# Kernel tuning notes

Measured on AMD Instinct MI355X. Metric: run time of the kernel, lower is better.

The kernel has to match this reference:

```python
import jax, jax.numpy as jnp
import numpy as np

NUM_HEAD = 8
HIDDEN = 1024


def setup_inputs() -> dict:
    key = jax.random.key(0)
    ks = jax.random.split(key, 7)
    B, Q, K = 2, 256, 256
    return {
        "query": jax.random.normal(ks[0], (B, Q, HIDDEN), jnp.float32),
        "keys": jax.random.normal(ks[1], (B, K, HIDDEN), jnp.float32),
        "values": jax.random.normal(ks[2], (B, K, HIDDEN), jnp.float32),
        "mask": jax.random.randint(ks[3], (B, K), 0, 2, jnp.int32),
        "W_q": jax.random.normal(ks[4], (HIDDEN, HIDDEN), jnp.float32),
        "W_k": jax.random.normal(ks[5], (HIDDEN, HIDDEN), jnp.float32),
        "V_a": jax.random.normal(ks[6], (HIDDEN,), jnp.float32),
    }


def reference(query, keys, values, mask, W_q, W_k, V_a):
    B, Q, H = query.shape
    K = keys.shape[1]
    h_q = query @ W_q                                   # [B,Q,H]
    h_k = keys @ W_k                                    # [B,K,H]
    # additive (Bahdanau) scores, split hidden into heads and sum per head
    h = jnp.tanh(h_q[:, :, None, :] + h_k[:, None, :, :]) * V_a   # [B,Q,K,H]
    logits = h.reshape(B, Q, K, NUM_HEAD, H // NUM_HEAD).sum(-1)  # [B,Q,K,h]
    logits = jnp.transpose(logits, (0, 3, 1, 2))        # [B,h,Q,K]
    penalty = (1.0 - mask.astype(jnp.float32)) * 99.0   # [B,K]
    logits = logits - penalty[:, None, None, :]
    weights = jax.nn.softmax(logits, axis=-1)           # [B,h,Q,K]
    v = values.reshape(B, K, NUM_HEAD, H // NUM_HEAD)   # [B,K,h,d]
    ctx = jnp.einsum('bhqk,bkhd->bqhd', weights, v).reshape(B, Q, H)
    return ctx, weights
```

## Files before the change

### kernel.cpp

```cpp
#include <hip/hip_runtime.h>
#include <hip/hip_bf16.h>


#define TANH_SCALE 2.88539008177792681472f
#define LOG2E      1.44269504088896340736f
#define UCLAMP     13.0f

typedef __attribute__((ext_vector_type(8))) short bf16x8_t;
typedef __attribute__((ext_vector_type(4))) float f32x4_t;

__device__ inline ushort bf16_rne(float f) {
  unsigned u = __float_as_uint(f);
  u += 0x7FFFu + ((u >> 16) & 1u);
  return (ushort)(u >> 16);
}
__device__ inline float bf16_to_f(ushort h) { return __uint_as_float((unsigned)h << 16); }
__device__ inline void split1(float v, ushort& hi, ushort& lo) {
  hi = bf16_rne(v);
  lo = bf16_rne(v - bf16_to_f(hi));
}
__device__ inline float pow8c(float u) {
  u = fminf(u, UCLAMP);
  float u2 = u * u;
  float u4 = u2 * u2;
  return u4 * u4;
}

__global__ __launch_bounds__(256) void prep(
    const float* __restrict__ query, const float* __restrict__ keys,
    const float* __restrict__ Wq, const float* __restrict__ Wk,
    ushort* __restrict__ qhi, ushort* __restrict__ qlo,
    ushort* __restrict__ khi, ushort* __restrict__ klo,
    ushort* __restrict__ wqthi, ushort* __restrict__ wqtlo,
    ushort* __restrict__ wkthi, ushort* __restrict__ wktlo)
{
  __shared__ float t[64][65];
  const int bid = blockIdx.x, tid = threadIdx.x;
  if (bid < 1024) {
    const int z = bid >> 9;
    const float* in = z ? keys : query;
    ushort* hi = z ? khi : qhi;
    ushort* lo = z ? klo : qlo;
    const size_t i = ((size_t)(bid & 511) * 256 + tid) * 4;
    float4 v = *(const float4*)(in + i);
    ushort h0, h1, h2, h3, l0, l1, l2, l3;
    split1(v.x, h0, l0); split1(v.y, h1, l1);
    split1(v.z, h2, l2); split1(v.w, h3, l3);
    *(ushort4*)(hi + i) = make_ushort4(h0, h1, h2, h3);
    *(ushort4*)(lo + i) = make_ushort4(l0, l1, l2, l3);
  } else {
    const int idx = bid - 1024;
    const int z = idx >> 8;
    const float* W = z ? Wk : Wq;
    ushort* thi = z ? wkthi : wqthi;
    ushort* tlo = z ? wktlo : wqtlo;
    const int n0 = (idx & 15) * 64, h0 = ((idx >> 4) & 15) * 64;
    const int r = tid >> 4, c = (tid & 15) * 4;
#pragma unroll
    for (int i = 0; i < 4; ++i) {
      const int rr = r + i * 16;
      float4 wv = *(const float4*)(W + (size_t)(h0 + rr) * 1024 + n0 + c);
      t[rr][c + 0] = wv.x; t[rr][c + 1] = wv.y;
      t[rr][c + 2] = wv.z; t[rr][c + 3] = wv.w;
    }
    __syncthreads();
#pragma unroll
    for (int i = 0; i < 4; ++i) {
      const int rr = r + i * 16;
      ushort h0v, h1v, h2v, h3v, l0v, l1v, l2v, l3v;
      split1(t[c + 0][rr] * TANH_SCALE, h0v, l0v);
      split1(t[c + 1][rr] * TANH_SCALE, h1v, l1v);
      split1(t[c + 2][rr] * TANH_SCALE, h2v, l2v);
      split1(t[c + 3][rr] * TANH_SCALE, h3v, l3v);
      *(ushort4*)(thi + (size_t)(n0 + rr) * 1024 + h0 + c) = make_ushort4(h0v, h1v, h2v, h3v);
      *(ushort4*)(tlo + (size_t)(n0 + rr) * 1024 + h0 + c) = make_ushort4(l0v, l1v, l2v, l3v);
    }
  }
}

__global__ __launch_bounds__(256) void gemm_mfma(
    const ushort* __restrict__ qhi, const ushort* __restrict__ qlo,
    const ushort* __restrict__ khi, const ushort* __restrict__ klo,
    const ushort* __restrict__ wqthi, const ushort* __restrict__ wqtlo,
    const ushort* __restrict__ wkthi, const ushort* __restrict__ wktlo,
    float* __restrict__ GQ, float* __restrict__ GKT)
{
  const int z = blockIdx.y;
  const int bid = blockIdx.x;
  int m0, n0, ldc;
  const ushort *Ah_g, *Al_g, *Bh_g, *Bl_g;
  float* Gp;
  if (z == 0) {
    m0 = (bid >> 4) * 64; n0 = (bid & 15) * 64; ldc = 1024;
    Ah_g = qhi; Al_g = qlo; Bh_g = wqthi; Bl_g = wqtlo; Gp = GQ;
  } else {
    m0 = (bid >> 3) * 64; n0 = (bid & 7) * 64; ldc = 512;
    Ah_g = wkthi; Al_g = wktlo; Bh_g = khi; Bl_g = klo; Gp = GKT;
  }

  __shared__ __align__(16) ushort Ah[64 * 40];
  __shared__ __align__(16) ushort Al[64 * 40];
  __shared__ __align__(16) ushort Bh[64 * 40];
  __shared__ __align__(16) ushort Bl[64 * 40];

  const int tid = threadIdx.x;
  const int srow = tid >> 2, skc = (tid & 3) * 8;
  const size_t gA = (size_t)(m0 + srow) * 1024 + skc;
  const size_t gB = (size_t)(n0 + srow) * 1024 + skc;
  const int soff = srow * 40 + skc;

  uint4 rah = *(const uint4*)(Ah_g + gA);
  uint4 ral = *(const uint4*)(Al_g + gA);
  uint4 rbh = *(const uint4*)(Bh_g + gB);
  uint4 rbl = *(const uint4*)(Bl_g + gB);

  const int w = __builtin_amdgcn_readfirstlane(tid >> 6);
  const int lane = tid & 63;
  const int wm = (w >> 1) * 32, wn = (w & 1) * 32;
  const int fr = lane & 15, kg = lane >> 4;
  const int aoff = (wm + fr) * 40 + kg * 8;
  const int boff = (wn + fr) * 40 + kg * 8;

  f32x4_t acc[2][2] = {};

  for (int kk = 0; kk < 1024; kk += 32) {
    __syncthreads();
    *(uint4*)(Ah + soff) = rah;
    *(uint4*)(Al + soff) = ral;
    *(uint4*)(Bh + soff) = rbh;
    *(uint4*)(Bl + soff) = rbl;
    __syncthreads();

    if (kk + 32 < 1024) {
      rah = *(const uint4*)(Ah_g + gA + kk + 32);
      ral = *(const uint4*)(Al_g + gA + kk + 32);
      rbh = *(const uint4*)(Bh_g + gB + kk + 32);
      rbl = *(const uint4*)(Bl_g + gB + kk + 32);
    }

    bf16x8_t ah0 = *(const bf16x8_t*)(Ah + aoff);
    bf16x8_t ah1 = *(const bf16x8_t*)(Ah + aoff + 16 * 40);
    bf16x8_t al0 = *(const bf16x8_t*)(Al + aoff);
    bf16x8_t al1 = *(const bf16x8_t*)(Al + aoff + 16 * 40);
    bf16x8_t bh0 = *(const bf16x8_t*)(Bh + boff);
    bf16x8_t bh1 = *(const bf16x8_t*)(Bh + boff + 16 * 40);
    bf16x8_t bl0 = *(const bf16x8_t*)(Bl + boff);
    bf16x8_t bl1 = *(const bf16x8_t*)(Bl + boff + 16 * 40);

    acc[0][0] = __builtin_amdgcn_mfma_f32_16x16x32_bf16(ah0, bh0, acc[0][0], 0, 0, 0);
    acc[0][1] = __builtin_amdgcn_mfma_f32_16x16x32_bf16(ah0, bh1, acc[0][1], 0, 0, 0);
    acc[1][0] = __builtin_amdgcn_mfma_f32_16x16x32_bf16(ah1, bh0, acc[1][0], 0, 0, 0);
    acc[1][1] = __builtin_amdgcn_mfma_f32_16x16x32_bf16(ah1, bh1, acc[1][1], 0, 0, 0);
    acc[0][0] = __builtin_amdgcn_mfma_f32_16x16x32_bf16(ah0, bl0, acc[0][0], 0, 0, 0);
    acc[0][1] = __builtin_amdgcn_mfma_f32_16x16x32_bf16(ah0, bl1, acc[0][1], 0, 0, 0);
    acc[1][0] = __builtin_amdgcn_mfma_f32_16x16x32_bf16(ah1, bl0, acc[1][0], 0, 0, 0);
    acc[1][1] = __builtin_amdgcn_mfma_f32_16x16x32_bf16(ah1, bl1, acc[1][1], 0, 0, 0);
    acc[0][0] = __builtin_amdgcn_mfma_f32_16x16x32_bf16(al0, bh0, acc[0][0], 0, 0, 0);
    acc[0][1] = __builtin_amdgcn_mfma_f32_16x16x32_bf16(al0, bh1, acc[0][1], 0, 0, 0);
    acc[1][0] = __builtin_amdgcn_mfma_f32_16x16x32_bf16(al1, bh0, acc[1][0], 0, 0, 0);
    acc[1][1] = __builtin_amdgcn_mfma_f32_16x16x32_bf16(al1, bh1, acc[1][1], 0, 0, 0);
  }

#pragma unroll
  for (int fm = 0; fm < 2; ++fm)
#pragma unroll
    for (int fn = 0; fn < 2; ++fn) {
      const int col = n0 + wn + fn * 16 + fr;
#pragma unroll
      for (int j = 0; j < 4; ++j) {
        const int row = m0 + wm + fm * 16 + kg * 4 + j;
        Gp[(size_t)row * ldc + col] = __builtin_amdgcn_exp2f(acc[fm][fn][j] * 0.125f);
      }
    }
}

__global__ __launch_bounds__(512) void attn_fused(
    const float* __restrict__ GQ, const float* __restrict__ GKT,
    const float* __restrict__ Va, const int* __restrict__ mask,
    const float* __restrict__ values,
    float* __restrict__ weights, float* __restrict__ ctx)
{
  __shared__ __align__(16) float gq_s[8][128];
  __shared__ __align__(16) float va_s[128];
  __shared__ __align__(16) float acc_lds[4][64][8];
  __shared__ float red_m[4][8];
  __shared__ float red_s[4][8];
  __shared__ __align__(16) float P_lds[8][256];
  __shared__ __align__(16) float4 pv_part[4][2][32];

  const int tid = threadIdx.x;
  const int lane = tid & 63;
  const int w = __builtin_amdgcn_readfirstlane(tid >> 6);
  const int bid = blockIdx.x;
  const int bh = bid >> 5;
  const int b = bh & 1, h = bh >> 1;
  const int qt = (bid & 31) * 8;
  const int dh = w >> 2, kq = w & 3;
  const int k = kq * 64 + lane;

  {
    const int i2 = tid * 2;
    const int sq = i2 >> 7, sd = i2 & 127;
    *(float2*)&gq_s[sq][sd] =
        *(const float2*)(GQ + (size_t)(b * 256 + qt + sq) * 1024 + h * 128 + sd);
    if (tid < 32) *(float4*)&va_s[tid * 4] = *(const float4*)(Va + h * 128 + tid * 4);
  }

  const float pen = 99.0f * (1.0f - (float)mask[b * 256 + k]);

  float ssum = Va[h * 128 + lane] + Va[h * 128 + 64 + lane];
#pragma unroll
  for (int off = 32; off; off >>= 1) ssum += __shfl_xor(ssum, off, 64);

  const float* gkp = GKT + (size_t)(h * 128 + dh * 64) * 512 + b * 256 + k;

  __syncthreads();

  float acc[8] = {0.f, 0.f, 0.f, 0.f, 0.f, 0.f, 0.f, 0.f};

  float gkc[8];
#pragma unroll
  for (int j = 0; j < 8; ++j) gkc[j] = gkp[(size_t)j * 512];

  for (int ch = 0; ch < 8; ++ch) {
    const int d0 = ch * 8;
    float gkn[8];
    if (ch < 7) {
#pragma unroll
      for (int j = 0; j < 8; ++j) gkn[j] = gkp[(size_t)(d0 + 8 + j) * 512];
    }
    float va_[8];
    *(float4*)&va_[0] = *(const float4*)&va_s[dh * 64 + d0];
    *(float4*)&va_[4] = *(const float4*)&va_s[dh * 64 + d0 + 4];
    const float s01 = va_[0] + va_[1], s23 = va_[2] + va_[3];
    const float s45 = va_[4] + va_[5], s67 = va_[6] + va_[7];
#pragma unroll
    for (int q = 0; q < 8; ++q) {
      float gqr[8];
      *(float4*)&gqr[0] = *(const float4*)&gq_s[q][dh * 64 + d0];
      *(float4*)&gqr[4] = *(const float4*)&gq_s[q][dh * 64 + d0 + 4];
      {
        const float t0 = pow8c(gqr[0] * gkc[0]);
        const float t1 = pow8c(gqr[1] * gkc[1]);
        const float t2 = pow8c(gqr[2] * gkc[2]);
        const float t3 = pow8c(gqr[3] * gkc[3]);
        const float p01 = fmaf(t0, t1, t0 + t1 + 1.0f);
        const float p23 = fmaf(t2, t3, t2 + t3 + 1.0f);
        const float den = p01 * p23;
        const float n01 = fmaf(va_[0], t1, fmaf(va_[1], t0, s01));
        const float n23 = fmaf(va_[2], t3, fmaf(va_[3], t2, s23));
        const float N = fmaf(n01, p23, n23 * p01);
        acc[q] = fmaf(N, __builtin_amdgcn_rcpf(den), acc[q]);
      }
      {
        const float t0 = pow8c(gqr[4] * gkc[4]);
        const float t1 = pow8c(gqr[5] * gkc[5]);
        const float t2 = pow8c(gqr[6] * gkc[6]);
        const float t3 = pow8c(gqr[7] * gkc[7]);
        const float p01 = fmaf(t0, t1, t0 + t1 + 1.0f);
        const float p23 = fmaf(t2, t3, t2 + t3 + 1.0f);
        const float den = p01 * p23;
        const float n01 = fmaf(va_[4], t1, fmaf(va_[5], t0, s45));
        const float n23 = fmaf(va_[6], t3, fmaf(va_[7], t2, s67));
        const float N = fmaf(n01, p23, n23 * p01);
        acc[q] = fmaf(N, __builtin_amdgcn_rcpf(den), acc[q]);
      }
    }
    if (ch < 7) {
#pragma unroll
      for (int j = 0; j < 8; ++j) gkc[j] = gkn[j];
    }
  }

  if (w >= 4) {
#pragma unroll
    for (int q = 0; q < 8; ++q) acc_lds[kq][lane][q] = acc[q];
  }
  __syncthreads();

  float l[8], p[8];
  if (w < 4) {
#pragma unroll
    for (int q = 0; q < 8; ++q) {
      acc[q] += acc_lds[kq][lane][q];
      l[q] = ssum - 2.0f * acc[q] - pen;
    }
#pragma unroll
    for (int q = 0; q < 8; ++q) {
      float m = l[q];
#pragma unroll
      for (int off = 32; off; off >>= 1) m = fmaxf(m, __shfl_xor(m, off, 64));
      if (lane == 0) red_m[w][q] = m;
    }
  }
  __syncthreads();
  if (w < 4) {
#pragma unroll
    for (int q = 0; q < 8; ++q) {
      float m = fmaxf(fmaxf(red_m[0][q], red_m[1][q]), fmaxf(red_m[2][q], red_m[3][q]));
      p[q] = __builtin_amdgcn_exp2f((l[q] - m) * LOG2E);
    }
#pragma unroll
    for (int q = 0; q < 8; ++q) {
      float s = p[q];
#pragma unroll
      for (int off = 32; off; off >>= 1) s += __shfl_xor(s, off, 64);
      if (lane == 0) red_s[w][q] = s;
    }
  }
  __syncthreads();
  if (w < 4) {
#pragma unroll
    for (int q = 0; q < 8; ++q) {
      const float s = (red_s[0][q] + red_s[1][q]) + (red_s[2][q] + red_s[3][q]);
      const float pq = p[q] / s;
      weights[((size_t)((b * 8 + h) * 256) + qt + q) * 256 + k] = pq;
      P_lds[q][k] = pq;
    }
  }
  __syncthreads();

  {
    const int rp = w & 3, kh = w >> 2;
    const int d4 = lane & 31, ks = lane >> 5;
    const int q0 = rp * 2, q1 = q0 + 1;
    const float* vb = values + (size_t)(b * 256 + kh * 128 + ks * 64) * 1024 + h * 128 + d4 * 4;
    const float* w0p = &P_lds[q0][kh * 128 + ks * 64];
    const float* w1p = &P_lds[q1][kh * 128 + ks * 64];
    float4 A0 = make_float4(0, 0, 0, 0), A1 = make_float4(0, 0, 0, 0);
#pragma unroll 4
    for (int j = 0; j < 64; ++j) {
      float4 v = *(const float4*)(vb + (size_t)j * 1024);
      const float pw0 = w0p[j], pw1 = w1p[j];
      A0.x += pw0 * v.x; A0.y += pw0 * v.y; A0.z += pw0 * v.z; A0.w += pw0 * v.w;
      A1.x += pw1 * v.x; A1.y += pw1 * v.y; A1.z += pw1 * v.z; A1.w += pw1 * v.w;
    }
    A0.x += __shfl_xor(A0.x, 32, 64); A0.y += __shfl_xor(A0.y, 32, 64);
    A0.z += __shfl_xor(A0.z, 32, 64); A0.w += __shfl_xor(A0.w, 32, 64);
    A1.x += __shfl_xor(A1.x, 32, 64); A1.y += __shfl_xor(A1.y, 32, 64);
    A1.z += __shfl_xor(A1.z, 32, 64); A1.w += __shfl_xor(A1.w, 32, 64);
    if (w >= 4 && lane < 32) {
      pv_part[rp][0][d4] = A0;
      pv_part[rp][1][d4] = A1;
    }
    __syncthreads();
    if (w < 4 && lane < 32) {
      float4 pa = pv_part[rp][0][d4];
      float4 pb = pv_part[rp][1][d4];
      A0.x += pa.x; A0.y += pa.y; A0.z += pa.z; A0.w += pa.w;
      A1.x += pb.x; A1.y += pb.y; A1.z += pb.z; A1.w += pb.w;
      *(float4*)&ctx[(size_t)(b * 256 + qt + q0) * 1024 + h * 128 + d4 * 4] = A0;
      *(float4*)&ctx[(size_t)(b * 256 + qt + q1) * 1024 + h * 128 + d4 * 4] = A1;
    }
  }
}

extern "C" void kernel_launch(void* const* d_in, const int* in_sizes, int n_in,
                              void* d_out, int out_size, void* d_ws, size_t ws_size,
                              hipStream_t stream) {
  const float* query  = (const float*)d_in[0];
  const float* keys   = (const float*)d_in[1];
  const float* values = (const float*)d_in[2];
  const int*   mask   = (const int*)d_in[3];
  const float* Wq     = (const float*)d_in[4];
  const float* Wk     = (const float*)d_in[5];
  const float* Va     = (const float*)d_in[6];

  float* ctx     = (float*)d_out;
  float* weights = ctx + 524288;

  ushort* qhi   = (ushort*)d_ws;
  ushort* qlo   = qhi + 524288;
  ushort* khi   = qlo + 524288;
  ushort* klo   = khi + 524288;
  ushort* wqthi = klo + 524288;
  ushort* wqtlo = wqthi + 1048576;
  ushort* wkthi = wqtlo + 1048576;
  ushort* wktlo = wkthi + 1048576;
  float*  GQ    = (float*)(wktlo + 1048576);
  float*  GKT   = GQ + 524288;

  prep<<<dim3(1536), 256, 0, stream>>>(query, keys, Wq, Wk,
                                       qhi, qlo, khi, klo,
                                       wqthi, wqtlo, wkthi, wktlo);
  gemm_mfma<<<dim3(128, 2), 256, 0, stream>>>(qhi, qlo, khi, klo,
                                              wqthi, wqtlo, wkthi, wktlo, GQ, GKT);
  attn_fused<<<dim3(512), 512, 0, stream>>>(GQ, GKT, Va, mask, values, weights, ctx);
}
```

Baseline: 66.28 us.

## Halve query tile per block, double grid, and pack tanh-score math into float2 vectors

The attention kernel now handles 4 query rows per block instead of 8, doubling the grid to 1024 blocks. It also restructures the P·V split across 4 key quarters with a 4-way LDS reduction. The rational tanh-score arithmetic is packed into two-wide float vectors so it can use packed FP32 ops, and the launch bounds ask for higher occupancy. More blocks means the per-block GK column loads and softmax overhead are repeated twice as often, trading redundant global traffic for more parallelism and shorter per-block latency.

```diff
diff --git a/kernel.cpp b/kernel.cpp
--- a/kernel.cpp
+++ b/kernel.cpp
@@ -8,6 +8,7 @@
 
 typedef __attribute__((ext_vector_type(8))) short bf16x8_t;
 typedef __attribute__((ext_vector_type(4))) float f32x4_t;
+typedef __attribute__((ext_vector_type(2))) float f32x2;
 
 __device__ inline ushort bf16_rne(float f) {
   unsigned u = __float_as_uint(f);
@@ -18,12 +19,6 @@
 __device__ inline void split1(float v, ushort& hi, ushort& lo) {
   hi = bf16_rne(v);
   lo = bf16_rne(v - bf16_to_f(hi));
-}
-__device__ inline float pow8c(float u) {
-  u = fminf(u, UCLAMP);
-  float u2 = u * u;
-  float u4 = u2 * u2;
-  return u4 * u4;
 }
 
 __global__ __launch_bounds__(256) void prep(
@@ -174,37 +169,33 @@
     }
 }
 
-__global__ __launch_bounds__(512) void attn_fused(
+__global__ __launch_bounds__(512, 8) void attn_fused(
     const float* __restrict__ GQ, const float* __restrict__ GKT,
     const float* __restrict__ Va, const int* __restrict__ mask,
     const float* __restrict__ values,
     float* __restrict__ weights, float* __restrict__ ctx)
 {
-  __shared__ __align__(16) float gq_s[8][128];
+  __shared__ __align__(16) float gq_s[4][128];
   __shared__ __align__(16) float va_s[128];
-  __shared__ __align__(16) float acc_lds[4][64][8];
-  __shared__ float red_m[4][8];
-  __shared__ float red_s[4][8];
-  __shared__ __align__(16) float P_lds[8][256];
-  __shared__ __align__(16) float4 pv_part[4][2][32];
+  __shared__ __align__(16) float acc_lds[4][64][4];
+  __shared__ float red_m[4][4];
+  __shared__ float red_s[4][4];
+  __shared__ __align__(16) float P_lds[4][256];
+  __shared__ __align__(16) float4 pv_part[4][2][2][32];
 
   const int tid = threadIdx.x;
   const int lane = tid & 63;
   const int w = __builtin_amdgcn_readfirstlane(tid >> 6);
   const int bid = blockIdx.x;
-  const int bh = bid >> 5;
+  const int bh = bid >> 6;
   const int b = bh & 1, h = bh >> 1;
-  const int qt = (bid & 31) * 8;
+  const int qt = (bid & 63) * 4;
   const int dh = w >> 2, kq = w & 3;
   const int k = kq * 64 + lane;
 
-  {
-    const int i2 = tid * 2;
-    const int sq = i2 >> 7, sd = i2 & 127;
-    *(float2*)&gq_s[sq][sd] =
-        *(const float2*)(GQ + (size_t)(b * 256 + qt + sq) * 1024 + h * 128 + sd);
-    if (tid < 32) *(float4*)&va_s[tid * 4] = *(const float4*)(Va + h * 128 + tid * 4);
-  }
+  gq_s[tid >> 7][tid & 127] =
+      GQ[(size_t)(b * 256 + qt + (tid >> 7)) * 1024 + h * 128 + (tid & 127)];
+  if (tid < 32) *(float4*)&va_s[tid * 4] = *(const float4*)(Va + h * 128 + tid * 4);
 
   const float pen = 99.0f * (1.0f - (float)mask[b * 256 + k]);
 
@@ -216,7 +207,9 @@
 
   __syncthreads();
 
-  float acc[8] = {0.f, 0.f, 0.f, 0.f, 0.f, 0.f, 0.f, 0.f};
+  const f32x2 ONE2 = {1.0f, 1.0f};
+  const f32x2 UC2 = {UCLAMP, UCLAMP};
+  f32x2 accv[4] = {{0.f, 0.f}, {0.f, 0.f}, {0.f, 0.f}, {0.f, 0.f}};
 
   float gkc[8];
 #pragma unroll
@@ -229,42 +222,36 @@
 #pragma unroll
       for (int j = 0; j < 8; ++j) gkn[j] = gkp[(size_t)(d0 + 8 + j) * 512];
     }
+    const f32x2 gk0 = {gkc[0], gkc[4]}, gk1 = {gkc[1], gkc[5]};
+    const f32x2 gk2 = {gkc[2], gkc[6]}, gk3 = {gkc[3], gkc[7]};
     float va_[8];
     *(float4*)&va_[0] = *(const float4*)&va_s[dh * 64 + d0];
     *(float4*)&va_[4] = *(const float4*)&va_s[dh * 64 + d0 + 4];
-    const float s01 = va_[0] + va_[1], s23 = va_[2] + va_[3];
-    const float s45 = va_[4] + va_[5], s67 = va_[6] + va_[7];
-#pragma unroll
-    for (int q = 0; q < 8; ++q) {
-      float gqr[8];
-      *(float4*)&gqr[0] = *(const float4*)&gq_s[q][dh * 64 + d0];
-      *(float4*)&gqr[4] = *(const float4*)&gq_s[q][dh * 64 + d0 + 4];
-      {
-        const float t0 = pow8c(gqr[0] * gkc[0]);
-        const float t1 = pow8c(gqr[1] * gkc[1]);
-        const float t2 = pow8c(gqr[2] * gkc[2]);
-        const float t3 = pow8c(gqr[3] * gkc[3]);
-        const float p01 = fmaf(t0, t1, t0 + t1 + 1.0f);
-        const float p23 = fmaf(t2, t3, t2 + t3 + 1.0f);
-        const float den = p01 * p23;
-        const float n01 = fmaf(va_[0], t1, fmaf(va_[1], t0, s01));
-        const float n23 = fmaf(va_[2], t3, fmaf(va_[3], t2, s23));
-        const float N = fmaf(n01, p23, n23 * p01);
-        acc[q] = fmaf(N, __builtin_amdgcn_rcpf(den), acc[q]);
-      }
-      {
-        const float t0 = pow8c(gqr[4] * gkc[4]);
-        const float t1 = pow8c(gqr[5] * gkc[5]);
-        const float t2 = pow8c(gqr[6] * gkc[6]);
-        const float t3 = pow8c(gqr[7] * gkc[7]);
-        const float p01 = fmaf(t0, t1, t0 + t1 + 1.0f);
-        const float p23 = fmaf(t2, t3, t2 + t3 + 1.0f);
-        const float den = p01 * p23;
-        const float n01 = fmaf(va_[4], t1, fmaf(va_[5], t0, s45));
-        const float n23 = fmaf(va_[6], t3, fmaf(va_[7], t2, s67));
-        const float N = fmaf(n01, p23, n23 * p01);
-        acc[q] = fmaf(N, __builtin_amdgcn_rcpf(den), acc[q]);
-      }
+    const f32x2 vp0 = {va_[0], va_[4]}, vp1 = {va_[1], va_[5]};
+    const f32x2 vp2 = {va_[2], va_[6]}, vp3 = {va_[3], va_[7]};
+    const f32x2 s01v = vp0 + vp1, s23v = vp2 + vp3;
+#pragma unroll
+    for (int q = 0; q < 4; ++q) {
+      float4 ga = *(const float4*)&gq_s[q][dh * 64 + d0];
+      float4 gb = *(const float4*)&gq_s[q][dh * 64 + d0 + 4];
+      f32x2 u0 = __builtin_elementwise_min((f32x2){ga.x, gb.x} * gk0, UC2);
+      f32x2 u1 = __builtin_elementwise_min((f32x2){ga.y, gb.y} * gk1, UC2);
+      f32x2 u2 = __builtin_elementwise_min((f32x2){ga.z, gb.z} * gk2, UC2);
+      f32x2 u3 = __builtin_elementwise_min((f32x2){ga.w, gb.w} * gk3, UC2);
+      u0 = u0 * u0; u1 = u1 * u1; u2 = u2 * u2; u3 = u3 * u3;
+      u0 = u0 * u0; u1 = u1 * u1; u2 = u2 * u2; u3 = u3 * u3;
+      const f32x2 t0 = u0 * u0, t1 = u1 * u1;
+      const f32x2 t2 = u2 * u2, t3 = u3 * u3;
+      const f32x2 p01 = t0 * t1 + (t0 + t1 + ONE2);
+      const f32x2 p23 = t2 * t3 + (t2 + t3 + ONE2);
+      const f32x2 den = p01 * p23;
+      const f32x2 n01 = vp0 * t1 + (vp1 * t0 + s01v);
+      const f32x2 n23 = vp2 * t3 + (vp3 * t2 + s23v);
+      const f32x2 Nv = n01 * p23 + n23 * p01;
+      f32x2 rv;
+      rv.x = __builtin_amdgcn_rcpf(den.x);
+      rv.y = __builtin_amdgcn_rcpf(den.y);
+      accv[q] = Nv * rv + accv[q];
     }
     if (ch < 7) {
 #pragma unroll
@@ -272,21 +259,25 @@
     }
   }
 
+  float acc[4];
+#pragma unroll
+  for (int q = 0; q < 4; ++q) acc[q] = accv[q].x + accv[q].y;
+
   if (w >= 4) {
 #pragma unroll
-    for (int q = 0; q < 8; ++q) acc_lds[kq][lane][q] = acc[q];
-  }
-  __syncthreads();
-
-  float l[8], p[8];
+    for (int q = 0; q < 4; ++q) acc_lds[kq][lane][q] = acc[q];
+  }
+  __syncthreads();
+
+  float l[4], p[4];
   if (w < 4) {
 #pragma unroll
-    for (int q = 0; q < 8; ++q) {
+    for (int q = 0; q < 4; ++q) {
       acc[q] += acc_lds[kq][lane][q];
       l[q] = ssum - 2.0f * acc[q] - pen;
     }
 #pragma unroll
-    for (int q = 0; q < 8; ++q) {
+    for (int q = 0; q < 4; ++q) {
       float m = l[q];
 #pragma unroll
       for (int off = 32; off; off >>= 1) m = fmaxf(m, __shfl_xor(m, off, 64));
@@ -296,12 +287,12 @@
   __syncthreads();
   if (w < 4) {
 #pragma unroll
-    for (int q = 0; q < 8; ++q) {
+    for (int q = 0; q < 4; ++q) {
       float m = fmaxf(fmaxf(red_m[0][q], red_m[1][q]), fmaxf(red_m[2][q], red_m[3][q]));
       p[q] = __builtin_amdgcn_exp2f((l[q] - m) * LOG2E);
     }
 #pragma unroll
-    for (int q = 0; q < 8; ++q) {
+    for (int q = 0; q < 4; ++q) {
       float s = p[q];
 #pragma unroll
       for (int off = 32; off; off >>= 1) s += __shfl_xor(s, off, 64);
@@ -311,7 +302,7 @@
   __syncthreads();
   if (w < 4) {
 #pragma unroll
-    for (int q = 0; q < 8; ++q) {
+    for (int q = 0; q < 4; ++q) {
       const float s = (red_s[0][q] + red_s[1][q]) + (red_s[2][q] + red_s[3][q]);
       const float pq = p[q] / s;
       weights[((size_t)((b * 8 + h) * 256) + qt + q) * 256 + k] = pq;
@@ -321,15 +312,16 @@
   __syncthreads();
 
   {
-    const int rp = w & 3, kh = w >> 2;
+    const int rp = w & 1, kq2 = w >> 1;
     const int d4 = lane & 31, ks = lane >> 5;
     const int q0 = rp * 2, q1 = q0 + 1;
-    const float* vb = values + (size_t)(b * 256 + kh * 128 + ks * 64) * 1024 + h * 128 + d4 * 4;
-    const float* w0p = &P_lds[q0][kh * 128 + ks * 64];
-    const float* w1p = &P_lds[q1][kh * 128 + ks * 64];
+    const float* vb =
+        values + (size_t)(b * 256 + kq2 * 64 + ks * 32) * 1024 + h * 128 + d4 * 4;
+    const float* w0p = &P_lds[q0][kq2 * 64 + ks * 32];
+    const float* w1p = &P_lds[q1][kq2 * 64 + ks * 32];
     float4 A0 = make_float4(0, 0, 0, 0), A1 = make_float4(0, 0, 0, 0);
 #pragma unroll 4
-    for (int j = 0; j < 64; ++j) {
+    for (int j = 0; j < 32; ++j) {
       float4 v = *(const float4*)(vb + (size_t)j * 1024);
       const float pw0 = w0p[j], pw1 = w1p[j];
       A0.x += pw0 * v.x; A0.y += pw0 * v.y; A0.z += pw0 * v.z; A0.w += pw0 * v.w;
@@ -339,16 +331,19 @@
     A0.z += __shfl_xor(A0.z, 32, 64); A0.w += __shfl_xor(A0.w, 32, 64);
     A1.x += __shfl_xor(A1.x, 32, 64); A1.y += __shfl_xor(A1.y, 32, 64);
     A1.z += __shfl_xor(A1.z, 32, 64); A1.w += __shfl_xor(A1.w, 32, 64);
-    if (w >= 4 && lane < 32) {
-      pv_part[rp][0][d4] = A0;
-      pv_part[rp][1][d4] = A1;
+    if (kq2 != 0 && lane < 32) {
+      pv_part[kq2][rp][0][d4] = A0;
+      pv_part[kq2][rp][1][d4] = A1;
     }
     __syncthreads();
-    if (w < 4 && lane < 32) {
-      float4 pa = pv_part[rp][0][d4];
-      float4 pb = pv_part[rp][1][d4];
-      A0.x += pa.x; A0.y += pa.y; A0.z += pa.z; A0.w += pa.w;
-      A1.x += pb.x; A1.y += pb.y; A1.z += pb.z; A1.w += pb.w;
+    if (kq2 == 0 && lane < 32) {
+#pragma unroll
+      for (int s = 1; s < 4; ++s) {
+        float4 pa = pv_part[s][rp][0][d4];
+        float4 pb = pv_part[s][rp][1][d4];
+        A0.x += pa.x; A0.y += pa.y; A0.z += pa.z; A0.w += pa.w;
+        A1.x += pb.x; A1.y += pb.y; A1.z += pb.z; A1.w += pb.w;
+      }
       *(float4*)&ctx[(size_t)(b * 256 + qt + q0) * 1024 + h * 128 + d4 * 4] = A0;
       *(float4*)&ctx[(size_t)(b * 256 + qt + q1) * 1024 + h * 128 + d4 * 4] = A1;
     }
@@ -385,5 +380,5 @@
                                        wqthi, wqtlo, wkthi, wktlo);
   gemm_mfma<<<dim3(128, 2), 256, 0, stream>>>(qhi, qlo, khi, klo,
                                               wqthi, wqtlo, wkthi, wktlo, GQ, GKT);
-  attn_fused<<<dim3(512), 512, 0, stream>>>(GQ, GKT, Va, mask, values, weights, ctx);
-}
+  attn_fused<<<dim3(1024), 512, 0, stream>>>(GQ, GKT, Va, mask, values, weights, ctx);
+}
```

New measurement: 66.68 us. No clear change (+0.6%).
